# Kernel optimization log

Measured on AMD Instinct MI355X. Metric: run time of the kernel, lower is better.

## Reference

```python
import jax, jax.numpy as jnp
import numpy as np

N = 10000       # nodes (= number of eigenpairs)
NFEAT = 512
NCLASS = 64     # hidden size of attention/FFN when norm='none'
HID = 128       # feat_encoder hidden
DIM = 32        # eig encoder hidden_dim
K = 10          # outer loop count of ParamNonHarmonicEncoding
NF = DIM // 2   # num_freq = 16
OMEGA = 50.0
DMIN = 0.25
NLAYER = 1


def _ln(x, g, b, eps=1e-5):
    m = jnp.mean(x, axis=-1, keepdims=True)
    v = jnp.mean((x - m) ** 2, axis=-1, keepdims=True)
    return g * (x - m) / jnp.sqrt(v + eps) + b


def setup_inputs() -> dict:
    key = jax.random.key(0)
    ks = jax.random.split(key, 32)
    f32 = jnp.float32
    def w(k, shape, s=0.05):
        return jax.random.normal(k, shape, dtype=f32) * s
    inp = {
        "e": jax.random.uniform(ks[0], (N,), dtype=f32),
        "u": jax.random.normal(ks[1], (N, N), dtype=f32) / np.float32(np.sqrt(N)),
        "x": jax.random.normal(ks[2], (N, NFEAT), dtype=f32),
        # feat_encoder: Linear(nfeat,hid) -> ReLU -> Linear(hid,nclass)
        "fe_w1": w(ks[3], (NFEAT, HID)), "fe_b1": jnp.zeros((HID,), f32),
        "fe_w2": w(ks[4], (HID, NCLASS)), "fe_b2": jnp.zeros((NCLASS,), f32),
        # ParamNonHarmonicEncoding
        "freq_deltas": jax.random.uniform(ks[5], (NF,), dtype=f32) * 0.5,
        "freq_bias": jnp.zeros((), f32),
        "readout_w": w(ks[6], (K, 1 + 2 * NF), 0.1),
        "readout_b": jnp.zeros((K,), f32),
        "alpha_w": w(ks[7], (K, 1), 0.3),   # nn.Linear(k,1,bias=False)
        # mha pre-norm
        "mha_ln_g": jnp.ones((NCLASS,), f32), "mha_ln_b": jnp.zeros((NCLASS,), f32),
        # Diff attention (H=1, hidden=nclass)
        "wq1": w(ks[8], (NCLASS, NCLASS)), "bq1": jnp.zeros((NCLASS,), f32),
        "wk1": w(ks[9], (NCLASS, NCLASS)), "bk1": jnp.zeros((NCLASS,), f32),
        "wq2": w(ks[10], (NCLASS, NCLASS)), "bq2": jnp.zeros((NCLASS,), f32),
        "wk2": w(ks[11], (NCLASS, NCLASS)), "bk2": jnp.zeros((NCLASS,), f32),
        "wv": w(ks[12], (NCLASS, NCLASS)), "bv": jnp.zeros((NCLASS,), f32),
        "lq1": w(ks[13], (NCLASS,), 0.1), "lk1": w(ks[14], (NCLASS,), 0.1),
        "lq2": w(ks[15], (NCLASS,), 0.1), "lk2": w(ks[16], (NCLASS,), 0.1),
        "attn_ln_g": jnp.ones((NCLASS,), f32), "attn_ln_b": jnp.zeros((NCLASS,), f32),
        "out_w": w(ks[17], (NCLASS, NCLASS)), "out_b": jnp.zeros((NCLASS,), f32),
        # gating
        "gate_ln_g": jnp.ones((3 * NCLASS,), f32), "gate_ln_b": jnp.zeros((3 * NCLASS,), f32),
        "gate_w": w(ks[18], (3 * NCLASS, 3)), "gate_b": jnp.zeros((3,), f32),
        # FFN
        "ffn_ln_g": jnp.ones((NCLASS,), f32), "ffn_ln_b": jnp.zeros((NCLASS,), f32),
        "ffn_w1": w(ks[19], (NCLASS, NCLASS)), "ffn_b1": jnp.zeros((NCLASS,), f32),
        "ffn_w2": w(ks[20], (NCLASS, NCLASS)), "ffn_b2": jnp.zeros((NCLASS,), f32),
    }
    return inp


def reference(e, u, x, fe_w1, fe_b1, fe_w2, fe_b2,
              freq_deltas, freq_bias, readout_w, readout_b, alpha_w,
              mha_ln_g, mha_ln_b,
              wq1, bq1, wk1, bk1, wq2, bq2, wk2, bk2, wv, bv,
              lq1, lk1, lq2, lk2, attn_ln_g, attn_ln_b, out_w, out_b,
              gate_ln_g, gate_ln_b, gate_w, gate_b,
              ffn_ln_g, ffn_ln_b, ffn_w1, ffn_b1, ffn_w2, ffn_b2):
    # feat encoder (all dropouts are 0 / eval mode)
    h = jnp.maximum(x @ fe_w1 + fe_b1, 0.0) @ fe_w2 + fe_b2          # [N, C]

    # ParamNonHarmonicEncoding, vectorized over the k powers
    deltas = jax.nn.softplus(freq_deltas) + DMIN
    freqs = jnp.cumsum(deltas) + freq_bias
    freqs = OMEGA * jnp.tanh(freqs / OMEGA)                           # [F]
    powers = e[:, None] ** jnp.arange(1, K + 1, dtype=e.dtype)        # [N, K]
    phase = powers[:, :, None] * freqs                                # [N, K, F]
    ns = jnp.asarray(NF ** 0.5, e.dtype)
    feat = jnp.concatenate(
        [jnp.ones_like(powers)[..., None], jnp.sin(phase) / ns, jnp.cos(phase) / ns],
        axis=-1)                                                      # [N, K, 1+2F]
    eig = jnp.einsum('nkf,kf->nk', feat, readout_w) + readout_b      # [N, K]
    new_e = eig @ alpha_w                                             # [N, 1]

    for layer in range(NLAYER):
        # spectral propagation: u @ diag-like(new_e) @ u^T @ h
        utx = u.T @ h                                                 # [N, C]
        h_fur = u @ (new_e * utx)                                     # [N, C]

        # differential linear attention
        mh = _ln(h, mha_ln_g, mha_ln_b)
        q1 = mh @ wq1 + bq1; k1 = mh @ wk1 + bk1
        q2 = mh @ wq2 + bq2; k2 = mh @ wk2 + bk2
        v = mh @ wv + bv
        k1v = k1.T @ v                                                # [C, C]
        k2v = k2.T @ v
        lam1 = jnp.exp(jnp.sum(lq1 * lk1))
        lam2 = jnp.exp(jnp.sum(lq2 * lk2))
        lam_init = 0.8 - 0.6 * float(np.exp(-0.3 * layer))
        lam_full = lam1 - lam2 + lam_init
        xa = q1 @ k1v - (q2 @ k2v) * lam_full
        xa = _ln(xa, attn_ln_g, attn_ln_b) * (1.0 - lam_init)
        mha_h = xa @ out_w + out_b                                    # [N, C]

        # gated mixing
        cat = jnp.concatenate([h, mha_h, h_fur], axis=-1)             # [N, 3C]
        g = jax.nn.softmax(_ln(cat, gate_ln_g, gate_ln_b) @ gate_w + gate_b, axis=-1)
        mix = h * g[:, 0:1] + mha_h * g[:, 1:2] + h_fur * g[:, 2:3]

        f = _ln(mix, ffn_ln_g, ffn_ln_b)
        f = jax.nn.gelu(f @ ffn_w1 + ffn_b1, approximate=False) @ ffn_w2 + ffn_b2
        h = mix + f
    return h
```

## Files before the change

kernel.cpp:

```cpp
#include <hip/hip_runtime.h>
#include <hip/hip_bf16.h>
#include <math.h>

#define NN 10000
#define J48 10048
#define CHUNKS 157
#define CPS 10
#define SPLITS 16

typedef __bf16 bf16;
typedef bf16 bf16x8 __attribute__((ext_vector_type(8)));
typedef float f32x4 __attribute__((ext_vector_type(4)));

__device__ __forceinline__ float wave_sum64(float v) {
#pragma unroll
  for (int m = 32; m >= 1; m >>= 1) v += __shfl_xor(v, m, 64);
  return v;
}

__global__ void prep_kernel(const float* __restrict__ w1, const float* __restrict__ w2,
                            const float* __restrict__ wq1, const float* __restrict__ wk1,
                            const float* __restrict__ wq2, const float* __restrict__ wk2,
                            const float* __restrict__ wvw,
                            const float* __restrict__ bq1, const float* __restrict__ bk1,
                            const float* __restrict__ bq2, const float* __restrict__ bk2,
                            const float* __restrict__ bvv,
                            const float* __restrict__ lq1, const float* __restrict__ lk1,
                            const float* __restrict__ lq2, const float* __restrict__ lk2,
                            const float* __restrict__ freq_deltas, const float* __restrict__ freq_bias,
                            bf16* __restrict__ w1T, bf16* __restrict__ w2T, bf16* __restrict__ qkvT,
                            float* __restrict__ bqkv, float* __restrict__ freqs, float* __restrict__ lamb) {
  int tid = blockIdx.x * blockDim.x + threadIdx.x;
  int nthr = gridDim.x * blockDim.x;
  for (int i = tid; i < 512 * 128; i += nthr) {
    int o = i >> 9, k = i & 511;
    w1T[i] = (bf16)w1[k * 128 + o];
  }
  for (int i = tid; i < 64 * 128; i += nthr) {
    int o = i >> 7, k = i & 127;
    w2T[i] = (bf16)w2[k * 64 + o];
  }
  for (int i = tid; i < 320 * 64; i += nthr) {
    int r = i >> 6, k = i & 63;
    const float* W = (r < 64) ? wq1 : (r < 128) ? wk1 : (r < 192) ? wq2 : (r < 256) ? wk2 : wvw;
    qkvT[i] = (bf16)W[k * 64 + (r & 63)];
  }
  for (int i = tid; i < 320; i += nthr) {
    const float* B = (i < 64) ? bq1 : (i < 128) ? bk1 : (i < 192) ? bq2 : (i < 256) ? bk2 : bvv;
    bqkv[i] = B[i & 63];
  }
  if (blockIdx.x == 0) {
    if (threadIdx.x == 0) {
      float acc = freq_bias[0];
      for (int f = 0; f < 16; f++) {
        acc += log1pf(expf(freq_deltas[f])) + 0.25f;
        freqs[f] = 50.0f * tanhf(acc * (1.0f / 50.0f));
      }
    }
    if (threadIdx.x >= 64 && threadIdx.x < 128) {
      int l = threadIdx.x - 64;
      float s1 = wave_sum64(lq1[l] * lk1[l]);
      float s2 = wave_sum64(lq2[l] * lk2[l]);
      if (l == 0) lamb[0] = expf(s1) - expf(s2) + 0.2f;
    }
  }
}

__global__ void newe_kernel(const float* __restrict__ e, const float* __restrict__ rw,
                            const float* __restrict__ rb, const float* __restrict__ aw,
                            const float* __restrict__ freqs, float* __restrict__ newe) {
  int n = blockIdx.x * blockDim.x + threadIdx.x;
  if (n >= NN) return;
  float fr[16];
#pragma unroll
  for (int f = 0; f < 16; f++) fr[f] = freqs[f];
  float ev = e[n], p = 1.0f, acc = 0.0f;
  for (int k = 0; k < 10; k++) {
    p *= ev;
    float s = rb[k] + rw[k * 33];
#pragma unroll
    for (int f = 0; f < 16; f++) {
      float ph = p * fr[f];
      s += 0.25f * (__sinf(ph) * rw[k * 33 + 1 + f] + __cosf(ph) * rw[k * 33 + 17 + f]);
    }
    acc += s * aw[k];
  }
  newe[n] = acc;
}

__global__ __launch_bounds__(256) void g1_kernel(const float* __restrict__ x, const bf16* __restrict__ w1T,
                                                 const float* __restrict__ b1, bf16* __restrict__ t1b) {
  __shared__ bf16 la[64][40];
  __shared__ bf16 lb[128][40];
  const int bm = blockIdx.x * 64;
  const int lane = threadIdx.x & 63, wvid = threadIdx.x >> 6;
  const int am = threadIdx.x >> 2, aseg = (threadIdx.x & 3) * 8;
  const int arow = bm + am;
  f32x4 acc[8] = {};
  float4 aLo, aHi;
  uint4 bChunk[2];
  auto fetchAll = [&](int k0) {
    if (arow < NN) {
      const float4* p = (const float4*)(x + (size_t)arow * 512 + k0 + aseg);
      aLo = p[0]; aHi = p[1];
    } else {
      aLo = make_float4(0.f, 0.f, 0.f, 0.f); aHi = aLo;
    }
#pragma unroll
    for (int r = 0; r < 2; r++) {
      int slot = threadIdx.x * 2 + r;
      int n = slot >> 2, seg = (slot & 3) * 8;
      bChunk[r] = *(const uint4*)(w1T + n * 512 + k0 + seg);
    }
  };
  auto store = [&]() {
    union { uint4 v; bf16 b[8]; } pk;
    float av[8] = {aLo.x, aLo.y, aLo.z, aLo.w, aHi.x, aHi.y, aHi.z, aHi.w};
#pragma unroll
    for (int t = 0; t < 8; t++) pk.b[t] = (bf16)av[t];
    *(uint4*)&la[am][aseg] = pk.v;
#pragma unroll
    for (int r = 0; r < 2; r++) {
      int slot = threadIdx.x * 2 + r;
      int n = slot >> 2, seg = (slot & 3) * 8;
      *(uint4*)&lb[n][seg] = bChunk[r];
    }
  };
  fetchAll(0);
  for (int k0 = 0; k0 < 512; k0 += 32) {
    store();
    if (k0 + 32 < 512) fetchAll(k0 + 32);
    __syncthreads();
    bf16x8 af = *(const bf16x8*)&la[wvid * 16 + (lane & 15)][(lane >> 4) * 8];
#pragma unroll
    for (int s = 0; s < 8; s++) {
      bf16x8 bfr = *(const bf16x8*)&lb[s * 16 + (lane & 15)][(lane >> 4) * 8];
      acc[s] = __builtin_amdgcn_mfma_f32_16x16x32_bf16(af, bfr, acc[s], 0, 0, 0);
    }
    __syncthreads();
  }
#pragma unroll
  for (int s = 0; s < 8; s++) {
    int col = s * 16 + (lane & 15);
    float bvv = b1[col];
#pragma unroll
    for (int r = 0; r < 4; r++) {
      int row = bm + wvid * 16 + (lane >> 4) * 4 + r;
      if (row < NN) {
        float v = acc[s][r] + bvv;
        t1b[(size_t)row * 128 + col] = (bf16)(v > 0.f ? v : 0.f);
      }
    }
  }
}

__global__ __launch_bounds__(256) void g2_kernel(const bf16* __restrict__ t1b, const bf16* __restrict__ w2T,
                                                 const float* __restrict__ b2, float* __restrict__ h,
                                                 bf16* __restrict__ hT) {
  __shared__ bf16 la[64][72];
  __shared__ bf16 lb[64][72];
  const int bm = blockIdx.x * 64;
  const int lane = threadIdx.x & 63, wvid = threadIdx.x >> 6;
  f32x4 acc[4] = {};
  for (int k0 = 0; k0 < 128; k0 += 64) {
#pragma unroll
    for (int r = 0; r < 2; r++) {
      int slot = threadIdx.x * 2 + r;
      int m = slot >> 3, seg = (slot & 7) * 8;
      int row = bm + m;
      uint4 val = make_uint4(0u, 0u, 0u, 0u);
      if (row < NN) val = *(const uint4*)(t1b + (size_t)row * 128 + k0 + seg);
      *(uint4*)&la[m][seg] = val;
      *(uint4*)&lb[m][seg] = *(const uint4*)(w2T + m * 128 + k0 + seg);
    }
    __syncthreads();
#pragma unroll
    for (int ks = 0; ks < 2; ks++) {
      bf16x8 af = *(const bf16x8*)&la[wvid * 16 + (lane & 15)][ks * 32 + (lane >> 4) * 8];
#pragma unroll
      for (int s = 0; s < 4; s++) {
        bf16x8 bfr = *(const bf16x8*)&lb[s * 16 + (lane & 15)][ks * 32 + (lane >> 4) * 8];
        acc[s] = __builtin_amdgcn_mfma_f32_16x16x32_bf16(af, bfr, acc[s], 0, 0, 0);
      }
    }
    __syncthreads();
  }
#pragma unroll
  for (int s = 0; s < 4; s++) {
    int col = s * 16 + (lane & 15);
    float bvv = b2[col];
#pragma unroll
    for (int r = 0; r < 4; r++) {
      int row = bm + wvid * 16 + (lane >> 4) * 4 + r;
      if (row < NN) {
        float v = acc[s][r] + bvv;
        h[(size_t)row * 64 + col] = v;
        hT[(size_t)col * NN + row] = (bf16)v;
      }
    }
  }
}

__global__ __launch_bounds__(256) void mhln_kernel(const float* __restrict__ h, const float* __restrict__ g,
                                                   const float* __restrict__ b, bf16* __restrict__ mh) {
  int row = blockIdx.x * 4 + (threadIdx.x >> 6);
  int lane = threadIdx.x & 63;
  if (row >= NN) return;
  float v = h[(size_t)row * 64 + lane];
  float m = wave_sum64(v) * (1.0f / 64.0f);
  float d = v - m;
  float var = wave_sum64(d * d) * (1.0f / 64.0f);
  mh[(size_t)row * 64 + lane] = (bf16)(g[lane] * d * rsqrtf(var + 1e-5f) + b[lane]);
}

__global__ __launch_bounds__(256) void qkv_kernel(const bf16* __restrict__ mh, const bf16* __restrict__ qkvT,
                                                  const float* __restrict__ bqkv,
                                                  bf16* __restrict__ qq, bf16* __restrict__ kv) {
  __shared__ bf16 la[64][72];
  __shared__ bf16 lb[320][72];
  const int bm = blockIdx.x * 64;
  const int lane = threadIdx.x & 63, wvid = threadIdx.x >> 6;
#pragma unroll
  for (int r = 0; r < 2; r++) {
    int slot = threadIdx.x * 2 + r;
    int m = slot >> 3, seg = (slot & 7) * 8;
    int row = bm + m;
    uint4 val = make_uint4(0u, 0u, 0u, 0u);
    if (row < NN) val = *(const uint4*)(mh + (size_t)row * 64 + seg);
    *(uint4*)&la[m][seg] = val;
  }
#pragma unroll
  for (int r = 0; r < 10; r++) {
    int slot = threadIdx.x * 10 + r;
    int n = slot >> 3, seg = (slot & 7) * 8;
    *(uint4*)&lb[n][seg] = *(const uint4*)(qkvT + n * 64 + seg);
  }
  __syncthreads();
  f32x4 acc[20] = {};
#pragma unroll
  for (int ks = 0; ks < 2; ks++) {
    bf16x8 af = *(const bf16x8*)&la[wvid * 16 + (lane & 15)][ks * 32 + (lane >> 4) * 8];
#pragma unroll
    for (int s = 0; s < 20; s++) {
      bf16x8 bfr = *(const bf16x8*)&lb[s * 16 + (lane & 15)][ks * 32 + (lane >> 4) * 8];
      acc[s] = __builtin_amdgcn_mfma_f32_16x16x32_bf16(af, bfr, acc[s], 0, 0, 0);
    }
  }
#pragma unroll
  for (int s = 0; s < 20; s++) {
    int col = s * 16 + (lane & 15);
    float bvv = bqkv[col];
    bf16* dst; int dc, stride;
    if (col < 64)       { dst = qq; dc = col;       stride = 128; }
    else if (col < 128) { dst = kv; dc = col - 64;  stride = 192; }
    else if (col < 192) { dst = qq; dc = col - 64;  stride = 128; }
    else                { dst = kv; dc = col - 128; stride = 192; }
#pragma unroll
    for (int r = 0; r < 4; r++) {
      int row = bm + wvid * 16 + (lane >> 4) * 4 + r;
      if (row < NN) dst[(size_t)row * stride + dc] = (bf16)(acc[s][r] + bvv);
    }
  }
}

__global__ __launch_bounds__(256) void r1_kernel(const bf16* __restrict__ kv, float* __restrict__ part) {
  int b = blockIdx.x;
  int c1 = threadIdx.x & 63, grp = threadIdx.x >> 6;
  int r0 = b * 40;
  float a1[16] = {}, a2[16] = {};
  for (int r = 0; r < 40; r++) {
    const bf16* rowp = kv + (size_t)(r0 + r) * 192;
    float k1 = (float)rowp[c1];
    float k2 = (float)rowp[64 + c1];
#pragma unroll
    for (int q = 0; q < 16; q++) {
      float vv = (float)rowp[128 + grp * 16 + q];
      a1[q] += k1 * vv; a2[q] += k2 * vv;
    }
  }
  float* p1 = part + ((size_t)(b * 2 + 0) * 64 + c1) * 64 + grp * 16;
  float* p2 = part + ((size_t)(b * 2 + 1) * 64 + c1) * 64 + grp * 16;
#pragma unroll
  for (int q = 0; q < 16; q++) { p1[q] = a1[q]; p2[q] = a2[q]; }
}

__global__ __launch_bounds__(256) void r2a_kernel(const float* __restrict__ part, float* __restrict__ part2) {
  int flat = blockIdx.x * 256 + threadIdx.x;
  int y = blockIdx.y;
  int b0 = y * 32, b1 = min(250, b0 + 32);
  float s = 0.f;
  for (int b = b0; b < b1; b++) s += part[(size_t)b * 8192 + flat];
  part2[(size_t)flat * 8 + y] = s;
}

__global__ void r2b_kernel(const float* __restrict__ part2, const float* __restrict__ lamb, bf16* __restrict__ Bt) {
  int flat = blockIdx.x * 256 + threadIdx.x;
  int mat = flat >> 12, rem = flat & 4095;
  int d = rem >> 6, c = rem & 63;
  f32x4 lo = *(const f32x4*)(part2 + (size_t)flat * 8);
  f32x4 hi = *(const f32x4*)(part2 + (size_t)flat * 8 + 4);
  float s = lo[0] + lo[1] + lo[2] + lo[3] + hi[0] + hi[1] + hi[2] + hi[3];
  float v = mat ? (-lamb[0] * s) : s;
  Bt[c * 128 + mat * 64 + d] = (bf16)v;
}

__global__ __launch_bounds__(256) void d_split_kernel(const float* __restrict__ u, const bf16* __restrict__ hT,
                                                      float* __restrict__ dpart) {
  __shared__ bf16 la[64][72];
  __shared__ bf16 lb[64][72];
  const int j0 = blockIdx.x * 64;
  const int sk = blockIdx.y;
  const int c0 = sk * CPS, c1e = min(CHUNKS, c0 + CPS);
  const int t = threadIdx.x;
  const int lane = t & 63, wv = t >> 6;
  const int jl = (t & 15) * 4;
  const int ir = (t >> 4) * 4;
  f32x4 acc[4] = {};
  uint4 aC[2];
  float4 bC[4];
  auto fetchAll = [&](int i0) {
#pragma unroll
    for (int r = 0; r < 2; r++) {
      int slot = t * 2 + r;
      int c = slot >> 3, seg = (slot & 7) * 8;
      int i = i0 + seg;
      if (i + 7 < NN) aC[r] = *(const uint4*)(hT + (size_t)c * NN + i);
      else {
        union { uint4 v; bf16 b[8]; } tu;
#pragma unroll
        for (int q = 0; q < 8; q++) tu.b[q] = (i + q < NN) ? hT[(size_t)c * NN + i + q] : (bf16)0.f;
        aC[r] = tu.v;
      }
    }
#pragma unroll
    for (int q = 0; q < 4; q++) {
      int i = i0 + ir + q;
      if (i < NN && (j0 + jl + 3) < NN) bC[q] = *(const float4*)(u + (size_t)i * NN + j0 + jl);
      else if (i < NN) {
        float tmp[4];
#pragma unroll
        for (int q2 = 0; q2 < 4; q2++) tmp[q2] = (j0 + jl + q2 < NN) ? u[(size_t)i * NN + j0 + jl + q2] : 0.f;
        bC[q] = make_float4(tmp[0], tmp[1], tmp[2], tmp[3]);
      } else bC[q] = make_float4(0.f, 0.f, 0.f, 0.f);
    }
  };
  auto storeAll = [&]() {
#pragma unroll
    for (int r = 0; r < 2; r++) {
      int slot = t * 2 + r;
      int c = slot >> 3, seg = (slot & 7) * 8;
      *(uint4*)&la[c][seg] = aC[r];
    }
#pragma unroll
    for (int q2 = 0; q2 < 4; q2++) {
      int j = jl + q2;
      int isw = ir ^ (((j >> 2) & 3) << 3);
      union { uint2 w; bf16 b[4]; } pk;
      pk.b[0] = (bf16)((float*)&bC[0])[q2];
      pk.b[1] = (bf16)((float*)&bC[1])[q2];
      pk.b[2] = (bf16)((float*)&bC[2])[q2];
      pk.b[3] = (bf16)((float*)&bC[3])[q2];
      *(uint2*)&lb[j][isw] = pk.w;
    }
  };
  fetchAll(c0 * 64);
  for (int ch = c0; ch < c1e; ch++) {
    storeAll();
    if (ch + 1 < c1e) fetchAll((ch + 1) * 64);
    __syncthreads();
#pragma unroll
    for (int ks = 0; ks < 2; ks++) {
      bf16x8 af = *(const bf16x8*)&la[wv * 16 + (lane & 15)][ks * 32 + (lane >> 4) * 8];
#pragma unroll
      for (int s = 0; s < 4; s++) {
        int j = s * 16 + (lane & 15);
        int ioff = (ks * 32 + (lane >> 4) * 8) ^ (((j >> 2) & 3) << 3);
        bf16x8 bfr = *(const bf16x8*)&lb[j][ioff];
        acc[s] = __builtin_amdgcn_mfma_f32_16x16x32_bf16(af, bfr, acc[s], 0, 0, 0);
      }
    }
    __syncthreads();
  }
#pragma unroll
  for (int s = 0; s < 4; s++) {
    int col = s * 16 + (lane & 15);
#pragma unroll
    for (int r = 0; r < 4; r++) {
      int c = wv * 16 + (lane >> 4) * 4 + r;
      dpart[((size_t)sk * 64 + c) * J48 + j0 + col] = acc[s][r];
    }
  }
}

__global__ void dred_kernel(const float* __restrict__ dpart, const float* __restrict__ newe,
                            bf16* __restrict__ wutxT) {
  int idx = blockIdx.x * 256 + threadIdx.x;
  int c = idx / 2512;
  int j = (idx - c * 2512) * 4;
  if (c >= 64 || j >= NN) return;
  f32x4 s = {};
  for (int sk = 0; sk < SPLITS; sk++)
    s += *(const f32x4*)(dpart + ((size_t)sk * 64 + c) * J48 + j);
  union { uint2 w; bf16 b[4]; } pk;
#pragma unroll
  for (int q = 0; q < 4; q++) pk.b[q] = (bf16)(newe[j + q] * s[q]);
  *(uint2*)&wutxT[(size_t)c * NN + j] = pk.w;
}

__global__ __launch_bounds__(256) void e_split_kernel(const float* __restrict__ u, const bf16* __restrict__ wutxT,
                                                      float* __restrict__ epart) {
  __shared__ bf16 la[64][72];
  __shared__ bf16 lb[64][72];
  const int bm = blockIdx.x * 64;
  const int sk = blockIdx.y;
  const int c0 = sk * CPS, c1e = min(CHUNKS, c0 + CPS);
  const int t = threadIdx.x;
  const int lane = t & 63, wv = t >> 6;
  const int mA = t >> 2, segA = (t & 3) * 16;
  const int mrow = bm + mA;
  f32x4 acc[4] = {};
  float4 aC[4];
  uint4 bC[2];
  auto fetchAll = [&](int j0) {
    int j = j0 + segA;
    if (mrow < NN && j + 15 < NN) {
      const float4* p = (const float4*)(u + (size_t)mrow * NN + j);
      aC[0] = p[0]; aC[1] = p[1]; aC[2] = p[2]; aC[3] = p[3];
    } else {
#pragma unroll
      for (int q = 0; q < 4; q++) {
        float tmp[4];
#pragma unroll
        for (int q2 = 0; q2 < 4; q2++) {
          int jj = j + q * 4 + q2;
          tmp[q2] = (mrow < NN && jj < NN) ? u[(size_t)mrow * NN + jj] : 0.f;
        }
        aC[q] = make_float4(tmp[0], tmp[1], tmp[2], tmp[3]);
      }
    }
#pragma unroll
    for (int r = 0; r < 2; r++) {
      int slot = t * 2 + r;
      int c = slot >> 3, seg = (slot & 7) * 8;
      int jj = j0 + seg;
      if (jj + 7 < NN) bC[r] = *(const uint4*)(wutxT + (size_t)c * NN + jj);
      else {
        union { uint4 v; bf16 b[8]; } tu;
#pragma unroll
        for (int q = 0; q < 8; q++) tu.b[q] = (jj + q < NN) ? wutxT[(size_t)c * NN + jj + q] : (bf16)0.f;
        bC[r] = tu.v;
      }
    }
  };
  auto storeAll = [&]() {
    union { uint4 v[2]; bf16 b[16]; } pk;
#pragma unroll
    for (int q = 0; q < 4; q++)
#pragma unroll
      for (int q2 = 0; q2 < 4; q2++) pk.b[q * 4 + q2] = (bf16)((float*)&aC[q])[q2];
    *(uint4*)&la[mA][segA] = pk.v[0];
    *(uint4*)&la[mA][segA + 8] = pk.v[1];
#pragma unroll
    for (int r = 0; r < 2; r++) {
      int slot = t * 2 + r;
      int c = slot >> 3, seg = (slot & 7) * 8;
      *(uint4*)&lb[c][seg] = bC[r];
    }
  };
  fetchAll(c0 * 64);
  for (int ch = c0; ch < c1e; ch++) {
    storeAll();
    if (ch + 1 < c1e) fetchAll((ch + 1) * 64);
    __syncthreads();
#pragma unroll
    for (int ks = 0; ks < 2; ks++) {
      bf16x8 af = *(const bf16x8*)&la[wv * 16 + (lane & 15)][ks * 32 + (lane >> 4) * 8];
#pragma unroll
      for (int s = 0; s < 4; s++) {
        bf16x8 bfr = *(const bf16x8*)&lb[s * 16 + (lane & 15)][ks * 32 + (lane >> 4) * 8];
        acc[s] = __builtin_amdgcn_mfma_f32_16x16x32_bf16(af, bfr, acc[s], 0, 0, 0);
      }
    }
    __syncthreads();
  }
#pragma unroll
  for (int s = 0; s < 4; s++) {
    int col = s * 16 + (lane & 15);
#pragma unroll
    for (int r = 0; r < 4; r++) {
      int row = wv * 16 + (lane >> 4) * 4 + r;
      epart[((size_t)sk * J48 + bm + row) * 64 + col] = acc[s][r];
    }
  }
}

__global__ void ered_kernel(const float* __restrict__ epart, float* __restrict__ h_fur) {
  int idx = blockIdx.x * 256 + threadIdx.x;
  if (idx >= NN * 16) return;
  size_t off = (size_t)idx * 4;
  f32x4 s = {};
  for (int sk = 0; sk < SPLITS; sk++)
    s += *(const f32x4*)(epart + (size_t)sk * (J48 * 64) + off);
  *(f32x4*)(h_fur + off) = s;
}

__global__ __launch_bounds__(256) void hattn_kernel(const bf16* __restrict__ qq, const bf16* __restrict__ Bt,
                                                    const float* __restrict__ g, const float* __restrict__ b,
                                                    bf16* __restrict__ xan) {
  __shared__ bf16 la[64][136];
  __shared__ bf16 lb[64][136];
  const int bm = blockIdx.x * 64;
  const int lane = threadIdx.x & 63, wvid = threadIdx.x >> 6;
#pragma unroll
  for (int r = 0; r < 4; r++) {
    int slot = threadIdx.x * 4 + r;
    int m = slot >> 4, seg = (slot & 15) * 8;
    int row = bm + m;
    uint4 val = make_uint4(0u, 0u, 0u, 0u);
    if (row < NN) val = *(const uint4*)(qq + (size_t)row * 128 + seg);
    *(uint4*)&la[m][seg] = val;
    *(uint4*)&lb[m][seg] = *(const uint4*)(Bt + m * 128 + seg);
  }
  __syncthreads();
  f32x4 acc[4] = {};
#pragma unroll
  for (int ks = 0; ks < 4; ks++) {
    bf16x8 af = *(const bf16x8*)&la[wvid * 16 + (lane & 15)][ks * 32 + (lane >> 4) * 8];
#pragma unroll
    for (int s = 0; s < 4; s++) {
      bf16x8 bfr = *(const bf16x8*)&lb[s * 16 + (lane & 15)][ks * 32 + (lane >> 4) * 8];
      acc[s] = __builtin_amdgcn_mfma_f32_16x16x32_bf16(af, bfr, acc[s], 0, 0, 0);
    }
  }
#pragma unroll
  for (int r = 0; r < 4; r++) {
    float psum = acc[0][r] + acc[1][r] + acc[2][r] + acc[3][r];
#pragma unroll
    for (int msk = 1; msk < 16; msk <<= 1) psum += __shfl_xor(psum, msk, 64);
    float mean = psum * (1.0f / 64.0f);
    float pvar = 0.f;
#pragma unroll
    for (int s = 0; s < 4; s++) { float dd = acc[s][r] - mean; pvar += dd * dd; }
#pragma unroll
    for (int msk = 1; msk < 16; msk <<= 1) pvar += __shfl_xor(pvar, msk, 64);
    float rsq = rsqrtf(pvar * (1.0f / 64.0f) + 1e-5f);
    int row = bm + wvid * 16 + (lane >> 4) * 4 + r;
    if (row < NN) {
#pragma unroll
      for (int s = 0; s < 4; s++) {
        int col = s * 16 + (lane & 15);
        float o = 0.8f * (g[col] * (acc[s][r] - mean) * rsq + b[col]);
        xan[(size_t)row * 64 + col] = (bf16)o;
      }
    }
  }
}

__global__ __launch_bounds__(256) void final_kernel(const float* __restrict__ h, const float* __restrict__ h_fur,
                                                    const bf16* __restrict__ xan,
                                                    const float* __restrict__ out_w, const float* __restrict__ out_b,
                                                    const float* __restrict__ gg, const float* __restrict__ gb,
                                                    const float* __restrict__ gw, const float* __restrict__ gbias,
                                                    const float* __restrict__ fg, const float* __restrict__ fb,
                                                    const float* __restrict__ fw1, const float* __restrict__ fb1,
                                                    const float* __restrict__ fw2, const float* __restrict__ fb2,
                                                    float* __restrict__ out) {
  __shared__ float s_ow[64][64];
  __shared__ float s_w1[64][64];
  __shared__ float s_w2[64][64];
  __shared__ float s_gw[192][3];
  __shared__ float s_row[4][64];
  const int lane = threadIdx.x & 63, wvid = threadIdx.x >> 6;
  for (int i = threadIdx.x; i < 4096; i += 256) {
    ((float*)s_ow)[i] = out_w[i];
    ((float*)s_w1)[i] = fw1[i];
    ((float*)s_w2)[i] = fw2[i];
  }
  for (int i = threadIdx.x; i < 576; i += 256) ((float*)s_gw)[i] = gw[i];
  const int row = blockIdx.x * 4 + wvid;
  float x_h = h[(size_t)row * 64 + lane];
  float x_f = h_fur[(size_t)row * 64 + lane];
  float x_a = (float)xan[(size_t)row * 64 + lane];
  s_row[wvid][lane] = x_a;
  __syncthreads();
  float mha = out_b[lane];
#pragma unroll 8
  for (int d = 0; d < 64; d++) mha += s_row[wvid][d] * s_ow[d][lane];
  float m3 = wave_sum64(x_h + mha + x_f) * (1.0f / 192.0f);
  float dh = x_h - m3, dm = mha - m3, df = x_f - m3;
  float v3 = wave_sum64(dh * dh + dm * dm + df * df) * (1.0f / 192.0f);
  float rs3 = rsqrtf(v3 + 1e-5f);
  float l0 = gg[lane] * dh * rs3 + gb[lane];
  float l1 = gg[64 + lane] * dm * rs3 + gb[64 + lane];
  float l2 = gg[128 + lane] * df * rs3 + gb[128 + lane];
  float p0 = l0 * s_gw[lane][0] + l1 * s_gw[64 + lane][0] + l2 * s_gw[128 + lane][0];
  float p1 = l0 * s_gw[lane][1] + l1 * s_gw[64 + lane][1] + l2 * s_gw[128 + lane][1];
  float p2 = l0 * s_gw[lane][2] + l1 * s_gw[64 + lane][2] + l2 * s_gw[128 + lane][2];
  p0 = wave_sum64(p0) + gbias[0];
  p1 = wave_sum64(p1) + gbias[1];
  p2 = wave_sum64(p2) + gbias[2];
  float mx = fmaxf(p0, fmaxf(p1, p2));
  float e0 = expf(p0 - mx), e1 = expf(p1 - mx), e2 = expf(p2 - mx);
  float inv = 1.0f / (e0 + e1 + e2);
  float mix = x_h * (e0 * inv) + mha * (e1 * inv) + x_f * (e2 * inv);
  float mf = wave_sum64(mix) * (1.0f / 64.0f);
  float dmx = mix - mf;
  float vf = wave_sum64(dmx * dmx) * (1.0f / 64.0f);
  float f = fg[lane] * dmx * rsqrtf(vf + 1e-5f) + fb[lane];
  __syncthreads();
  s_row[wvid][lane] = f;
  __syncthreads();
  float t1 = fb1[lane];
#pragma unroll 8
  for (int d = 0; d < 64; d++) t1 += s_row[wvid][d] * s_w1[d][lane];
  t1 = 0.5f * t1 * (1.0f + erff(t1 * 0.70710678118654752f));
  __syncthreads();
  s_row[wvid][lane] = t1;
  __syncthreads();
  float f2 = fb2[lane];
#pragma unroll 8
  for (int d = 0; d < 64; d++) f2 += s_row[wvid][d] * s_w2[d][lane];
  out[(size_t)row * 64 + lane] = mix + f2;
}

extern "C" void kernel_launch(void* const* d_in, const int* in_sizes, int n_in,
                              void* d_out, int out_size, void* d_ws, size_t ws_size,
                              hipStream_t stream) {
  const float* e          = (const float*)d_in[0];
  const float* u          = (const float*)d_in[1];
  const float* x          = (const float*)d_in[2];
  const float* fe_w1      = (const float*)d_in[3];
  const float* fe_b1      = (const float*)d_in[4];
  const float* fe_w2      = (const float*)d_in[5];
  const float* fe_b2      = (const float*)d_in[6];
  const float* freq_deltas= (const float*)d_in[7];
  const float* freq_bias  = (const float*)d_in[8];
  const float* readout_w  = (const float*)d_in[9];
  const float* readout_b  = (const float*)d_in[10];
  const float* alpha_w    = (const float*)d_in[11];
  const float* mha_ln_g   = (const float*)d_in[12];
  const float* mha_ln_b   = (const float*)d_in[13];
  const float* wq1        = (const float*)d_in[14];
  const float* bq1        = (const float*)d_in[15];
  const float* wk1        = (const float*)d_in[16];
  const float* bk1        = (const float*)d_in[17];
  const float* wq2        = (const float*)d_in[18];
  const float* bq2        = (const float*)d_in[19];
  const float* wk2        = (const float*)d_in[20];
  const float* bk2        = (const float*)d_in[21];
  const float* wv_in      = (const float*)d_in[22];
  const float* bv_in      = (const float*)d_in[23];
  const float* lq1        = (const float*)d_in[24];
  const float* lk1        = (const float*)d_in[25];
  const float* lq2        = (const float*)d_in[26];
  const float* lk2        = (const float*)d_in[27];
  const float* attn_ln_g  = (const float*)d_in[28];
  const float* attn_ln_b  = (const float*)d_in[29];
  const float* out_w      = (const float*)d_in[30];
  const float* out_b      = (const float*)d_in[31];
  const float* gate_ln_g  = (const float*)d_in[32];
  const float* gate_ln_b  = (const float*)d_in[33];
  const float* gate_w     = (const float*)d_in[34];
  const float* gate_b     = (const float*)d_in[35];
  const float* ffn_ln_g   = (const float*)d_in[36];
  const float* ffn_ln_b   = (const float*)d_in[37];
  const float* ffn_w1     = (const float*)d_in[38];
  const float* ffn_b1     = (const float*)d_in[39];
  const float* ffn_w2     = (const float*)d_in[40];
  const float* ffn_b2     = (const float*)d_in[41];

  constexpr size_t OFF_H     = 0;
  constexpr size_t OFF_T1B   = 2560000;
  constexpr size_t OFF_HT    = 5120000;
  constexpr size_t OFF_MH    = 6400000;
  constexpr size_t OFF_QQ    = 7680000;
  constexpr size_t OFF_KV    = 10240000;
  constexpr size_t OFF_WUTXT = 14080000;
  constexpr size_t OFF_HFUR  = 15360000;
  constexpr size_t OFF_XAN   = 17920000;
  constexpr size_t OFF_NEWE  = 19200000;
  constexpr size_t OFF_BT    = 19240064;
  constexpr size_t OFF_W1T   = 19256448;
  constexpr size_t OFF_W2T   = 19387520;
  constexpr size_t OFF_QKVT  = 19403904;
  constexpr size_t OFF_BQKV  = 19444864;
  constexpr size_t OFF_FREQS = 19446144;
  constexpr size_t OFF_LAM   = 19446208;
  constexpr size_t OFF_BIG   = 19446272;
  constexpr size_t OFF_PART2 = OFF_BIG + 8192000;
  constexpr size_t WS_NEED   = OFF_BIG + (size_t)SPLITS * J48 * 64 * 4;
  if (ws_size < WS_NEED) return;

  char* ws = (char*)d_ws;
  float* h_buf   = (float*)(ws + OFF_H);
  bf16*  t1b     = (bf16*)(ws + OFF_T1B);
  bf16*  hT      = (bf16*)(ws + OFF_HT);
  bf16*  mh      = (bf16*)(ws + OFF_MH);
  bf16*  qq      = (bf16*)(ws + OFF_QQ);
  bf16*  kv      = (bf16*)(ws + OFF_KV);
  bf16*  wutxT   = (bf16*)(ws + OFF_WUTXT);
  float* h_fur   = (float*)(ws + OFF_HFUR);
  bf16*  xan     = (bf16*)(ws + OFF_XAN);
  float* newe    = (float*)(ws + OFF_NEWE);
  bf16*  Bt      = (bf16*)(ws + OFF_BT);
  bf16*  w1T     = (bf16*)(ws + OFF_W1T);
  bf16*  w2T     = (bf16*)(ws + OFF_W2T);
  bf16*  qkvT    = (bf16*)(ws + OFF_QKVT);
  float* bqkv    = (float*)(ws + OFF_BQKV);
  float* freqs   = (float*)(ws + OFF_FREQS);
  float* lamb    = (float*)(ws + OFF_LAM);
  float* part    = (float*)(ws + OFF_BIG);
  float* part2   = (float*)(ws + OFF_PART2);
  float* spart   = (float*)(ws + OFF_BIG);

  prep_kernel<<<64, 256, 0, stream>>>(fe_w1, fe_w2, wq1, wk1, wq2, wk2, wv_in,
                                      bq1, bk1, bq2, bk2, bv_in,
                                      lq1, lk1, lq2, lk2, freq_deltas, freq_bias,
                                      w1T, w2T, qkvT, bqkv, freqs, lamb);
  newe_kernel<<<40, 256, 0, stream>>>(e, readout_w, readout_b, alpha_w, freqs, newe);
  g1_kernel<<<157, 256, 0, stream>>>(x, w1T, fe_b1, t1b);
  g2_kernel<<<157, 256, 0, stream>>>(t1b, w2T, fe_b2, h_buf, hT);
  mhln_kernel<<<2500, 256, 0, stream>>>(h_buf, mha_ln_g, mha_ln_b, mh);
  qkv_kernel<<<157, 256, 0, stream>>>(mh, qkvT, bqkv, qq, kv);
  r1_kernel<<<250, 256, 0, stream>>>(kv, part);
  r2a_kernel<<<dim3(32, 8), 256, 0, stream>>>(part, part2);
  r2b_kernel<<<32, 256, 0, stream>>>(part2, lamb, Bt);
  d_split_kernel<<<dim3(157, SPLITS), 256, 0, stream>>>(u, hT, spart);
  dred_kernel<<<628, 256, 0, stream>>>(spart, newe, wutxT);
  e_split_kernel<<<dim3(157, SPLITS), 256, 0, stream>>>(u, wutxT, spart);
  ered_kernel<<<625, 256, 0, stream>>>(spart, h_fur);
  hattn_kernel<<<157, 256, 0, stream>>>(qq, Bt, attn_ln_g, attn_ln_b, xan);
  final_kernel<<<2500, 256, 0, stream>>>(h_buf, h_fur, xan, out_w, out_b,
                                         gate_ln_g, gate_ln_b, gate_w, gate_b,
                                         ffn_ln_g, ffn_ln_b, ffn_w1, ffn_b1, ffn_w2, ffn_b2,
                                         (float*)d_out);
}
```

Before: 366.2 us.

## Retile the u-streaming GEMMs, fuse the mha LayerNorm into g2, rebalance r1 reduction

The two big passes over the 10000x10000 u matrix are retiled. The d pass now uses 128-wide j tiles with a 32-deep k-step and 13 splits. The e pass uses 32-row tiles with a 128-deep k-step and 8 splits, which cuts the partial-sum traffic and the reduction work. The standalone mha LayerNorm kernel is folded into the g2 GEMM epilogue using cross-lane shuffles, removing one launch and a reread of h. r1 now runs on more, smaller blocks with vectorized v loads to spread the k^T v reduction across more CUs.

```diff
diff --git a/kernel.cpp b/kernel.cpp
--- a/kernel.cpp
+++ b/kernel.cpp
@@ -4,9 +4,13 @@
 
 #define NN 10000
 #define J48 10048
-#define CHUNKS 157
-#define CPS 10
-#define SPLITS 16
+#define DJ 10112
+#define DSPLITS 13
+#define DCPS 24
+#define DCHUNKS 313
+#define ESPLITS 8
+#define ECPS 10
+#define ECHUNKS 79
 
 typedef __bf16 bf16;
 typedef bf16 bf16x8 __attribute__((ext_vector_type(8)));
@@ -155,8 +159,9 @@
 }
 
 __global__ __launch_bounds__(256) void g2_kernel(const bf16* __restrict__ t1b, const bf16* __restrict__ w2T,
-                                                 const float* __restrict__ b2, float* __restrict__ h,
-                                                 bf16* __restrict__ hT) {
+                                                 const float* __restrict__ b2, const float* __restrict__ lng,
+                                                 const float* __restrict__ lnb, float* __restrict__ h,
+                                                 bf16* __restrict__ hT, bf16* __restrict__ mh) {
   __shared__ bf16 la[64][72];
   __shared__ bf16 lb[64][72];
   const int bm = blockIdx.x * 64;
@@ -185,32 +190,38 @@
     }
     __syncthreads();
   }
+  float bv4[4], g4[4], lb4[4];
 #pragma unroll
   for (int s = 0; s < 4; s++) {
     int col = s * 16 + (lane & 15);
-    float bvv = b2[col];
-#pragma unroll
-    for (int r = 0; r < 4; r++) {
-      int row = bm + wvid * 16 + (lane >> 4) * 4 + r;
-      if (row < NN) {
-        float v = acc[s][r] + bvv;
+    bv4[s] = b2[col]; g4[s] = lng[col]; lb4[s] = lnb[col];
+  }
+#pragma unroll
+  for (int r = 0; r < 4; r++) {
+    float vals[4], psum = 0.f;
+#pragma unroll
+    for (int s = 0; s < 4; s++) { vals[s] = acc[s][r] + bv4[s]; psum += vals[s]; }
+#pragma unroll
+    for (int msk = 1; msk < 16; msk <<= 1) psum += __shfl_xor(psum, msk, 64);
+    float mean = psum * (1.0f / 64.0f);
+    float pvar = 0.f;
+#pragma unroll
+    for (int s = 0; s < 4; s++) { float dd = vals[s] - mean; pvar += dd * dd; }
+#pragma unroll
+    for (int msk = 1; msk < 16; msk <<= 1) pvar += __shfl_xor(pvar, msk, 64);
+    float rsq = rsqrtf(pvar * (1.0f / 64.0f) + 1e-5f);
+    int row = bm + wvid * 16 + (lane >> 4) * 4 + r;
+    if (row < NN) {
+#pragma unroll
+      for (int s = 0; s < 4; s++) {
+        int col = s * 16 + (lane & 15);
+        float v = vals[s];
         h[(size_t)row * 64 + col] = v;
         hT[(size_t)col * NN + row] = (bf16)v;
-      }
-    }
-  }
-}
-
-__global__ __launch_bounds__(256) void mhln_kernel(const float* __restrict__ h, const float* __restrict__ g,
-                                                   const float* __restrict__ b, bf16* __restrict__ mh) {
-  int row = blockIdx.x * 4 + (threadIdx.x >> 6);
-  int lane = threadIdx.x & 63;
-  if (row >= NN) return;
-  float v = h[(size_t)row * 64 + lane];
-  float m = wave_sum64(v) * (1.0f / 64.0f);
-  float d = v - m;
-  float var = wave_sum64(d * d) * (1.0f / 64.0f);
-  mh[(size_t)row * 64 + lane] = (bf16)(g[lane] * d * rsqrtf(var + 1e-5f) + b[lane]);
+        mh[(size_t)row * 64 + col] = (bf16)(g4[s] * (v - mean) * rsq + lb4[s]);
+      }
+    }
+  }
 }
 
 __global__ __launch_bounds__(256) void qkv_kernel(const bf16* __restrict__ mh, const bf16* __restrict__ qkvT,
@@ -266,20 +277,24 @@
 __global__ __launch_bounds__(256) void r1_kernel(const bf16* __restrict__ kv, float* __restrict__ part) {
   int b = blockIdx.x;
   int c1 = threadIdx.x & 63, grp = threadIdx.x >> 6;
-  int r0 = b * 40;
+  int r0 = b * 16;
   float a1[16] = {}, a2[16] = {};
-  for (int r = 0; r < 40; r++) {
+  for (int r = 0; r < 16; r++) {
     const bf16* rowp = kv + (size_t)(r0 + r) * 192;
     float k1 = (float)rowp[c1];
     float k2 = (float)rowp[64 + c1];
-#pragma unroll
-    for (int q = 0; q < 16; q++) {
-      float vv = (float)rowp[128 + grp * 16 + q];
-      a1[q] += k1 * vv; a2[q] += k2 * vv;
-    }
-  }
-  float* p1 = part + ((size_t)(b * 2 + 0) * 64 + c1) * 64 + grp * 16;
-  float* p2 = part + ((size_t)(b * 2 + 1) * 64 + c1) * 64 + grp * 16;
+    union { uint4 v; bf16 b[8]; } v0, v1;
+    v0.v = *(const uint4*)(rowp + 128 + grp * 16);
+    v1.v = *(const uint4*)(rowp + 136 + grp * 16);
+#pragma unroll
+    for (int q = 0; q < 8; q++) {
+      float va = (float)v0.b[q], vb = (float)v1.b[q];
+      a1[q] += k1 * va; a2[q] += k2 * va;
+      a1[8 + q] += k1 * vb; a2[8 + q] += k2 * vb;
+    }
+  }
+  float* p1 = part + (size_t)b * 8192 + (size_t)c1 * 64 + grp * 16;
+  float* p2 = p1 + 4096;
 #pragma unroll
   for (int q = 0; q < 16; q++) { p1[q] = a1[q]; p2[q] = a2[q]; }
 }
@@ -287,7 +302,7 @@
 __global__ __launch_bounds__(256) void r2a_kernel(const float* __restrict__ part, float* __restrict__ part2) {
   int flat = blockIdx.x * 256 + threadIdx.x;
   int y = blockIdx.y;
-  int b0 = y * 32, b1 = min(250, b0 + 32);
+  int b0 = y * 79, b1 = min(625, b0 + 79);
   float s = 0.f;
   for (int b = b0; b < b1; b++) s += part[(size_t)b * 8192 + flat];
   part2[(size_t)flat * 8 + y] = s;
@@ -304,151 +319,134 @@
   Bt[c * 128 + mat * 64 + d] = (bf16)v;
 }
 
-__global__ __launch_bounds__(256) void d_split_kernel(const float* __restrict__ u, const bf16* __restrict__ hT,
-                                                      float* __restrict__ dpart) {
-  __shared__ bf16 la[64][72];
-  __shared__ bf16 lb[64][72];
-  const int j0 = blockIdx.x * 64;
+__global__ __launch_bounds__(256, 4) void d2_kernel(const float* __restrict__ u, const bf16* __restrict__ hT,
+                                                    float* __restrict__ dpart) {
+  __shared__ bf16 la[64][40];
+  __shared__ bf16 lb[128][40];
+  const int j0 = blockIdx.x * 128;
   const int sk = blockIdx.y;
-  const int c0 = sk * CPS, c1e = min(CHUNKS, c0 + CPS);
+  const int c0 = sk * DCPS;
+  const int c1e = min(DCHUNKS, c0 + DCPS + (sk == DSPLITS - 1 ? 1 : 0));
   const int t = threadIdx.x;
   const int lane = t & 63, wv = t >> 6;
-  const int jl = (t & 15) * 4;
-  const int ir = (t >> 4) * 4;
-  f32x4 acc[4] = {};
-  uint4 aC[2];
-  float4 bC[4];
+  const int hc = t >> 2, hseg = (t & 3) * 8;
+  const int ig = t >> 5;
+  const int jg = t & 31;
+  f32x4 acc[4][2] = {};
+  uint4 hC;
+  float4 uC[4];
   auto fetchAll = [&](int i0) {
-#pragma unroll
-    for (int r = 0; r < 2; r++) {
-      int slot = t * 2 + r;
-      int c = slot >> 3, seg = (slot & 7) * 8;
-      int i = i0 + seg;
-      if (i + 7 < NN) aC[r] = *(const uint4*)(hT + (size_t)c * NN + i);
+    {
+      int i = i0 + hseg;
+      if (i + 7 < NN) hC = *(const uint4*)(hT + (size_t)hc * NN + i);
       else {
         union { uint4 v; bf16 b[8]; } tu;
 #pragma unroll
-        for (int q = 0; q < 8; q++) tu.b[q] = (i + q < NN) ? hT[(size_t)c * NN + i + q] : (bf16)0.f;
-        aC[r] = tu.v;
-      }
-    }
+        for (int q = 0; q < 8; q++) tu.b[q] = (i + q < NN) ? hT[(size_t)hc * NN + i + q] : (bf16)0.f;
+        hC = tu.v;
+      }
+    }
+    int jj = j0 + jg * 4;
 #pragma unroll
     for (int q = 0; q < 4; q++) {
-      int i = i0 + ir + q;
-      if (i < NN && (j0 + jl + 3) < NN) bC[q] = *(const float4*)(u + (size_t)i * NN + j0 + jl);
-      else if (i < NN) {
-        float tmp[4];
-#pragma unroll
-        for (int q2 = 0; q2 < 4; q2++) tmp[q2] = (j0 + jl + q2 < NN) ? u[(size_t)i * NN + j0 + jl + q2] : 0.f;
-        bC[q] = make_float4(tmp[0], tmp[1], tmp[2], tmp[3]);
-      } else bC[q] = make_float4(0.f, 0.f, 0.f, 0.f);
+      int i = i0 + ig * 4 + q;
+      uC[q] = (i < NN && jj < NN) ? *(const float4*)(u + (size_t)i * NN + jj)
+                                  : make_float4(0.f, 0.f, 0.f, 0.f);
     }
   };
   auto storeAll = [&]() {
-#pragma unroll
-    for (int r = 0; r < 2; r++) {
-      int slot = t * 2 + r;
-      int c = slot >> 3, seg = (slot & 7) * 8;
-      *(uint4*)&la[c][seg] = aC[r];
-    }
+    *(uint4*)&la[hc][hseg] = hC;
 #pragma unroll
     for (int q2 = 0; q2 < 4; q2++) {
-      int j = jl + q2;
-      int isw = ir ^ (((j >> 2) & 3) << 3);
+      int j = jg * 4 + q2;
+      int isw = (ig * 4) ^ (((j >> 2) & 3) << 3);
       union { uint2 w; bf16 b[4]; } pk;
-      pk.b[0] = (bf16)((float*)&bC[0])[q2];
-      pk.b[1] = (bf16)((float*)&bC[1])[q2];
-      pk.b[2] = (bf16)((float*)&bC[2])[q2];
-      pk.b[3] = (bf16)((float*)&bC[3])[q2];
+      pk.b[0] = (bf16)((float*)&uC[0])[q2];
+      pk.b[1] = (bf16)((float*)&uC[1])[q2];
+      pk.b[2] = (bf16)((float*)&uC[2])[q2];
+      pk.b[3] = (bf16)((float*)&uC[3])[q2];
       *(uint2*)&lb[j][isw] = pk.w;
     }
   };
-  fetchAll(c0 * 64);
+  fetchAll(c0 * 32);
   for (int ch = c0; ch < c1e; ch++) {
     storeAll();
-    if (ch + 1 < c1e) fetchAll((ch + 1) * 64);
+    if (ch + 1 < c1e) fetchAll((ch + 1) * 32);
     __syncthreads();
-#pragma unroll
-    for (int ks = 0; ks < 2; ks++) {
-      bf16x8 af = *(const bf16x8*)&la[wv * 16 + (lane & 15)][ks * 32 + (lane >> 4) * 8];
-#pragma unroll
-      for (int s = 0; s < 4; s++) {
-        int j = s * 16 + (lane & 15);
-        int ioff = (ks * 32 + (lane >> 4) * 8) ^ (((j >> 2) & 3) << 3);
-        bf16x8 bfr = *(const bf16x8*)&lb[j][ioff];
-        acc[s] = __builtin_amdgcn_mfma_f32_16x16x32_bf16(af, bfr, acc[s], 0, 0, 0);
-      }
+    bf16x8 af[4];
+#pragma unroll
+    for (int sm = 0; sm < 4; sm++)
+      af[sm] = *(const bf16x8*)&la[sm * 16 + (lane & 15)][(lane >> 4) * 8];
+#pragma unroll
+    for (int sn = 0; sn < 2; sn++) {
+      int j = wv * 32 + sn * 16 + (lane & 15);
+      int isw = ((lane >> 4) * 8) ^ (((j >> 2) & 3) << 3);
+      bf16x8 bfr = *(const bf16x8*)&lb[j][isw];
+#pragma unroll
+      for (int sm = 0; sm < 4; sm++)
+        acc[sm][sn] = __builtin_amdgcn_mfma_f32_16x16x32_bf16(af[sm], bfr, acc[sm][sn], 0, 0, 0);
     }
     __syncthreads();
   }
 #pragma unroll
-  for (int s = 0; s < 4; s++) {
-    int col = s * 16 + (lane & 15);
-#pragma unroll
-    for (int r = 0; r < 4; r++) {
-      int c = wv * 16 + (lane >> 4) * 4 + r;
-      dpart[((size_t)sk * 64 + c) * J48 + j0 + col] = acc[s][r];
-    }
-  }
+  for (int sm = 0; sm < 4; sm++)
+#pragma unroll
+    for (int sn = 0; sn < 2; sn++) {
+      int j = j0 + wv * 32 + sn * 16 + (lane & 15);
+#pragma unroll
+      for (int r = 0; r < 4; r++) {
+        int c = sm * 16 + (lane >> 4) * 4 + r;
+        dpart[((size_t)sk * 64 + c) * DJ + j] = acc[sm][sn][r];
+      }
+    }
 }
 
 __global__ void dred_kernel(const float* __restrict__ dpart, const float* __restrict__ newe,
                             bf16* __restrict__ wutxT) {
   int idx = blockIdx.x * 256 + threadIdx.x;
-  int c = idx / 2512;
-  int j = (idx - c * 2512) * 4;
+  int c = idx / 2528;
+  int j = (idx - c * 2528) * 4;
   if (c >= 64 || j >= NN) return;
   f32x4 s = {};
-  for (int sk = 0; sk < SPLITS; sk++)
-    s += *(const f32x4*)(dpart + ((size_t)sk * 64 + c) * J48 + j);
+  for (int sk = 0; sk < DSPLITS; sk++)
+    s += *(const f32x4*)(dpart + ((size_t)sk * 64 + c) * DJ + j);
   union { uint2 w; bf16 b[4]; } pk;
 #pragma unroll
   for (int q = 0; q < 4; q++) pk.b[q] = (bf16)(newe[j + q] * s[q]);
   *(uint2*)&wutxT[(size_t)c * NN + j] = pk.w;
 }
 
-__global__ __launch_bounds__(256) void e_split_kernel(const float* __restrict__ u, const bf16* __restrict__ wutxT,
-                                                      float* __restrict__ epart) {
-  __shared__ bf16 la[64][72];
-  __shared__ bf16 lb[64][72];
-  const int bm = blockIdx.x * 64;
+__global__ __launch_bounds__(256, 4) void e2_kernel(const float* __restrict__ u, const bf16* __restrict__ wutxT,
+                                                    float* __restrict__ epart) {
+  __shared__ bf16 la[32][136];
+  __shared__ bf16 lb[64][136];
+  const int bm = blockIdx.x * 32;
   const int sk = blockIdx.y;
-  const int c0 = sk * CPS, c1e = min(CHUNKS, c0 + CPS);
+  const int c0 = sk * ECPS, c1e = min(ECHUNKS, c0 + ECPS);
   const int t = threadIdx.x;
   const int lane = t & 63, wv = t >> 6;
-  const int mA = t >> 2, segA = (t & 3) * 16;
-  const int mrow = bm + mA;
-  f32x4 acc[4] = {};
-  float4 aC[4];
-  uint4 bC[2];
-  auto fetchAll = [&](int j0) {
-    int j = j0 + segA;
-    if (mrow < NN && j + 15 < NN) {
-      const float4* p = (const float4*)(u + (size_t)mrow * NN + j);
-      aC[0] = p[0]; aC[1] = p[1]; aC[2] = p[2]; aC[3] = p[3];
-    } else {
-#pragma unroll
-      for (int q = 0; q < 4; q++) {
-        float tmp[4];
-#pragma unroll
-        for (int q2 = 0; q2 < 4; q2++) {
-          int jj = j + q * 4 + q2;
-          tmp[q2] = (mrow < NN && jj < NN) ? u[(size_t)mrow * NN + jj] : 0.f;
-        }
-        aC[q] = make_float4(tmp[0], tmp[1], tmp[2], tmp[3]);
-      }
-    }
-#pragma unroll
-    for (int r = 0; r < 2; r++) {
-      int slot = t * 2 + r;
-      int c = slot >> 3, seg = (slot & 7) * 8;
-      int jj = j0 + seg;
-      if (jj + 7 < NN) bC[r] = *(const uint4*)(wutxT + (size_t)c * NN + jj);
+  const int ur = t >> 3, useg = (t & 7) * 16;
+  const int wc = t >> 2, wseg = (t & 3) * 32;
+  const int mrow = bm + ur;
+  f32x4 acc[2] = {};
+  float4 uC[4];
+  uint4 wC[4];
+  auto fetchAll = [&](int jc) {
+#pragma unroll
+    for (int q = 0; q < 4; q++) {
+      int j = jc + useg + q * 4;
+      uC[q] = (mrow < NN && j < NN) ? *(const float4*)(u + (size_t)mrow * NN + j)
+                                    : make_float4(0.f, 0.f, 0.f, 0.f);
+    }
+#pragma unroll
+    for (int q = 0; q < 4; q++) {
+      int j = jc + wseg + q * 8;
+      if (j + 7 < NN) wC[q] = *(const uint4*)(wutxT + (size_t)wc * NN + j);
       else {
         union { uint4 v; bf16 b[8]; } tu;
 #pragma unroll
-        for (int q = 0; q < 8; q++) tu.b[q] = (jj + q < NN) ? wutxT[(size_t)c * NN + jj + q] : (bf16)0.f;
-        bC[r] = tu.v;
+        for (int q2 = 0; q2 < 8; q2++) tu.b[q2] = (j + q2 < NN) ? wutxT[(size_t)wc * NN + j + q2] : (bf16)0.f;
+        wC[q] = tu.v;
       }
     }
   };
@@ -457,39 +455,35 @@
 #pragma unroll
     for (int q = 0; q < 4; q++)
 #pragma unroll
-      for (int q2 = 0; q2 < 4; q2++) pk.b[q * 4 + q2] = (bf16)((float*)&aC[q])[q2];
-    *(uint4*)&la[mA][segA] = pk.v[0];
-    *(uint4*)&la[mA][segA + 8] = pk.v[1];
-#pragma unroll
-    for (int r = 0; r < 2; r++) {
-      int slot = t * 2 + r;
-      int c = slot >> 3, seg = (slot & 7) * 8;
-      *(uint4*)&lb[c][seg] = bC[r];
-    }
+      for (int q2 = 0; q2 < 4; q2++) pk.b[q * 4 + q2] = (bf16)((float*)&uC[q])[q2];
+    *(uint4*)&la[ur][useg] = pk.v[0];
+    *(uint4*)&la[ur][useg + 8] = pk.v[1];
+#pragma unroll
+    for (int q = 0; q < 4; q++) *(uint4*)&lb[wc][wseg + q * 8] = wC[q];
   };
-  fetchAll(c0 * 64);
+  fetchAll(c0 * 128);
   for (int ch = c0; ch < c1e; ch++) {
     storeAll();
-    if (ch + 1 < c1e) fetchAll((ch + 1) * 64);
+    if (ch + 1 < c1e) fetchAll((ch + 1) * 128);
     __syncthreads();
 #pragma unroll
-    for (int ks = 0; ks < 2; ks++) {
-      bf16x8 af = *(const bf16x8*)&la[wv * 16 + (lane & 15)][ks * 32 + (lane >> 4) * 8];
-#pragma unroll
-      for (int s = 0; s < 4; s++) {
-        bf16x8 bfr = *(const bf16x8*)&lb[s * 16 + (lane & 15)][ks * 32 + (lane >> 4) * 8];
-        acc[s] = __builtin_amdgcn_mfma_f32_16x16x32_bf16(af, bfr, acc[s], 0, 0, 0);
+    for (int kk = 0; kk < 4; kk++) {
+      bf16x8 af = *(const bf16x8*)&la[(wv & 1) * 16 + (lane & 15)][kk * 32 + (lane >> 4) * 8];
+#pragma unroll
+      for (int sn = 0; sn < 2; sn++) {
+        bf16x8 bfr = *(const bf16x8*)&lb[(wv >> 1) * 32 + sn * 16 + (lane & 15)][kk * 32 + (lane >> 4) * 8];
+        acc[sn] = __builtin_amdgcn_mfma_f32_16x16x32_bf16(af, bfr, acc[sn], 0, 0, 0);
       }
     }
     __syncthreads();
   }
 #pragma unroll
-  for (int s = 0; s < 4; s++) {
-    int col = s * 16 + (lane & 15);
+  for (int sn = 0; sn < 2; sn++) {
+    int c = (wv >> 1) * 32 + sn * 16 + (lane & 15);
 #pragma unroll
     for (int r = 0; r < 4; r++) {
-      int row = wv * 16 + (lane >> 4) * 4 + r;
-      epart[((size_t)sk * J48 + bm + row) * 64 + col] = acc[s][r];
+      int i = bm + (wv & 1) * 16 + (lane >> 4) * 4 + r;
+      epart[((size_t)sk * J48 + i) * 64 + c] = acc[sn][r];
     }
   }
 }
@@ -499,7 +493,7 @@
   if (idx >= NN * 16) return;
   size_t off = (size_t)idx * 4;
   f32x4 s = {};
-  for (int sk = 0; sk < SPLITS; sk++)
+  for (int sk = 0; sk < ESPLITS; sk++)
     s += *(const f32x4*)(epart + (size_t)sk * (J48 * 64) + off);
   *(f32x4*)(h_fur + off) = s;
 }
@@ -687,8 +681,9 @@
   constexpr size_t OFF_FREQS = 19446144;
   constexpr size_t OFF_LAM   = 19446208;
   constexpr size_t OFF_BIG   = 19446272;
-  constexpr size_t OFF_PART2 = OFF_BIG + 8192000;
-  constexpr size_t WS_NEED   = OFF_BIG + (size_t)SPLITS * J48 * 64 * 4;
+  constexpr size_t OFF_PART2 = OFF_BIG + 20480000;
+  constexpr size_t SZ_DPART  = (size_t)DSPLITS * 64 * DJ * 4;
+  constexpr size_t WS_NEED   = OFF_BIG + SZ_DPART;
   if (ws_size < WS_NEED) return;
 
   char* ws = (char*)d_ws;
@@ -711,7 +706,8 @@
   float* lamb    = (float*)(ws + OFF_LAM);
   float* part    = (float*)(ws + OFF_BIG);
   float* part2   = (float*)(ws + OFF_PART2);
-  float* spart   = (float*)(ws + OFF_BIG);
+  float* dpart   = (float*)(ws + OFF_BIG);
+  float* epart   = (float*)(ws + OFF_BIG);
 
   prep_kernel<<<64, 256, 0, stream>>>(fe_w1, fe_w2, wq1, wk1, wq2, wk2, wv_in,
                                       bq1, bk1, bq2, bk2, bv_in,
@@ -719,16 +715,15 @@
                                       w1T, w2T, qkvT, bqkv, freqs, lamb);
   newe_kernel<<<40, 256, 0, stream>>>(e, readout_w, readout_b, alpha_w, freqs, newe);
   g1_kernel<<<157, 256, 0, stream>>>(x, w1T, fe_b1, t1b);
-  g2_kernel<<<157, 256, 0, stream>>>(t1b, w2T, fe_b2, h_buf, hT);
-  mhln_kernel<<<2500, 256, 0, stream>>>(h_buf, mha_ln_g, mha_ln_b, mh);
+  g2_kernel<<<157, 256, 0, stream>>>(t1b, w2T, fe_b2, mha_ln_g, mha_ln_b, h_buf, hT, mh);
   qkv_kernel<<<157, 256, 0, stream>>>(mh, qkvT, bqkv, qq, kv);
-  r1_kernel<<<250, 256, 0, stream>>>(kv, part);
+  r1_kernel<<<625, 256, 0, stream>>>(kv, part);
   r2a_kernel<<<dim3(32, 8), 256, 0, stream>>>(part, part2);
   r2b_kernel<<<32, 256, 0, stream>>>(part2, lamb, Bt);
-  d_split_kernel<<<dim3(157, SPLITS), 256, 0, stream>>>(u, hT, spart);
-  dred_kernel<<<628, 256, 0, stream>>>(spart, newe, wutxT);
-  e_split_kernel<<<dim3(157, SPLITS), 256, 0, stream>>>(u, wutxT, spart);
-  ered_kernel<<<625, 256, 0, stream>>>(spart, h_fur);
+  d2_kernel<<<dim3(79, DSPLITS), 256, 0, stream>>>(u, hT, dpart);
+  dred_kernel<<<632, 256, 0, stream>>>(dpart, newe, wutxT);
+  e2_kernel<<<dim3(313, ESPLITS), 256, 0, stream>>>(u, wutxT, epart);
+  ered_kernel<<<625, 256, 0, stream>>>(epart, h_fur);
   hattn_kernel<<<157, 256, 0, stream>>>(qq, Bt, attn_ln_g, attn_ln_b, xan);
   final_kernel<<<2500, 256, 0, stream>>>(h_buf, h_fur, xan, out_w, out_b,
                                          gate_ln_g, gate_ln_b, gate_w, gate_b,
```

After: 392.2 us. +7.1%, slower.
